# Performance work log

Hardware: AMD Instinct MI355X
Metric: run time of the kernel (lower is better)

## Reference

```python
import jax, jax.numpy as jnp
import numpy as np

D_MODEL = 1024
NHEAD = 16
HEAD_DIM = D_MODEL // NHEAD
EPS = 1e-5


def _layer_norm(x, gamma, beta):
    mu = jnp.mean(x, axis=-1, keepdims=True)
    var = jnp.mean(jnp.square(x - mu), axis=-1, keepdims=True)
    return (x - mu) * jax.lax.rsqrt(var + EPS) * gamma + beta


def setup_inputs() -> dict:
    key = jax.random.key(0)
    ks = jax.random.split(key, 8)
    s = 1.0 / np.sqrt(D_MODEL)
    return {
        "x": jax.random.normal(ks[0], (4, 2048, D_MODEL), dtype=jnp.float32),
        "Wq": jax.random.uniform(ks[1], (D_MODEL, D_MODEL), jnp.float32, -s, s),
        "Wk": jax.random.uniform(ks[2], (D_MODEL, D_MODEL), jnp.float32, -s, s),
        "Wv": jax.random.uniform(ks[3], (D_MODEL, D_MODEL), jnp.float32, -s, s),
        "ln1_g": jnp.ones((D_MODEL,), jnp.float32),
        "ln1_b": jnp.zeros((D_MODEL,), jnp.float32),
        "ln2_g": jnp.ones((D_MODEL,), jnp.float32),
        "ln2_b": jnp.zeros((D_MODEL,), jnp.float32),
        "W1": jax.random.uniform(ks[4], (D_MODEL, D_MODEL), jnp.float32, -s, s),
        "b1": jax.random.uniform(ks[5], (D_MODEL,), jnp.float32, -s, s),
        "W2": jax.random.uniform(ks[6], (D_MODEL, D_MODEL), jnp.float32, -s, s),
        "b2": jax.random.uniform(ks[7], (D_MODEL,), jnp.float32, -s, s),
    }


def reference(x, Wq, Wk, Wv, ln1_g, ln1_b, ln2_g, ln2_b, W1, b1, W2, b2):
    B, S, D = x.shape
    temperature = jnp.sqrt(jnp.asarray(D_MODEL / NHEAD, x.dtype))
    xn = _layer_norm(x, ln1_g, ln1_b)
    # torch Linear: y = x @ W.T (weights are [out, in], no bias for q/k/v)
    q = (xn @ Wq.T).reshape(B, S, NHEAD, HEAD_DIM)
    k = (xn @ Wk.T).reshape(B, S, NHEAD, HEAD_DIM)
    v = (xn @ Wv.T).reshape(B, S, NHEAD, HEAD_DIM)
    scores = jnp.einsum("bqhd,bkhd->bhqk", q, k) / temperature  # [B,H,S,S]
    causal = jnp.tril(jnp.ones((S, S), dtype=bool))
    scores = jnp.where(causal, scores, jnp.asarray(-jnp.inf, scores.dtype))
    attn = jax.nn.softmax(scores, axis=-1)
    att_out = jnp.einsum("bhqk,bkhd->bqhd", attn, v).reshape(B, S, D)
    xt = x + att_out
    xt2 = _layer_norm(xt, ln2_g, ln2_b)
    ffn = jax.nn.relu(xt2 @ W1.T + b1) @ W2.T + b2  # dropout=0 -> identity
    return xt + ffn
```

## Files before the change

### kernel.cpp

```cpp
#include <hip/hip_runtime.h>
#include <hip/hip_bf16.h>

typedef unsigned short u16;
typedef unsigned int u32;
typedef __attribute__((ext_vector_type(8))) __bf16 bf16x8;
typedef __attribute__((ext_vector_type(4))) float f32x4;
typedef __attribute__((ext_vector_type(8))) unsigned short ushort8v;
typedef __attribute__((ext_vector_type(4))) unsigned short u16x4;
typedef __attribute__((ext_vector_type(2))) unsigned int u32x2;

#define DEV __device__ __forceinline__
#define AS1 __attribute__((address_space(1)))
#define AS3 __attribute__((address_space(3)))

DEV u16 f2bf(float f) {
    union { float f; unsigned int i; } u; u.f = f;
    unsigned int x = u.i;
    unsigned int r = (x + 0x7fffu + ((x >> 16) & 1u)) >> 16;
    return (u16)r;
}
DEV float bf2f(u16 h) {
    union { unsigned int i; float f; } u; u.i = ((unsigned int)h) << 16;
    return u.f;
}
DEV u32 cvt_pk_bf16(float lo, float hi) {
    u32 r;
    asm("v_cvt_pk_bf16_f32 %0, %1, %2" : "=v"(r) : "v"(lo), "v"(hi));
    return r;
}

__global__ __launch_bounds__(256) void ln1_cvt(
    const float* __restrict__ xin,
    const float* __restrict__ g, const float* __restrict__ be,
    u16* __restrict__ y_bf,
    const float* __restrict__ wq, const float* __restrict__ wk,
    const float* __restrict__ wv, const float* __restrict__ w1,
    const float* __restrict__ w2, u16* __restrict__ wdst)
{
    const int tid = threadIdx.x;
    if (blockIdx.x >= 8192) {
        const int i = ((blockIdx.x - 8192) * 256 + tid) * 4;
        auto conv4 = [](float4 a) {
            u16x4 r; r[0] = f2bf(a.x); r[1] = f2bf(a.y); r[2] = f2bf(a.z); r[3] = f2bf(a.w);
            return r;
        };
        *(u16x4*)(wdst + i)               = conv4(*(const float4*)(wq + i));
        *(u16x4*)(wdst + (1 << 20) + i)   = conv4(*(const float4*)(wk + i));
        *(u16x4*)(wdst + (2 << 20) + i)   = conv4(*(const float4*)(wv + i));
        *(u16x4*)(wdst + (3 << 20) + i)   = conv4(*(const float4*)(w1 + i));
        *(u16x4*)(wdst + (4 << 20) + i)   = conv4(*(const float4*)(w2 + i));
        return;
    }
    const int row = blockIdx.x;
    const size_t base = (size_t)row * 1024 + tid * 4;
    float4 xv = *(const float4*)(xin + base);
    float v[4] = {xv.x, xv.y, xv.z, xv.w};
    float s = 0.f, ss = 0.f;
    #pragma unroll
    for (int j = 0; j < 4; ++j) { s += v[j]; ss += v[j] * v[j]; }
    #pragma unroll
    for (int o = 32; o > 0; o >>= 1) { s += __shfl_xor(s, o); ss += __shfl_xor(ss, o); }
    __shared__ float red[8];
    const int w = tid >> 6;
    if ((tid & 63) == 0) { red[w * 2] = s; red[w * 2 + 1] = ss; }
    __syncthreads();
    s  = red[0] + red[2] + red[4] + red[6];
    ss = red[1] + red[3] + red[5] + red[7];
    const float mu = s * (1.0f / 1024.0f);
    const float var = ss * (1.0f / 1024.0f) - mu * mu;
    const float rstd = rsqrtf(var + 1e-5f);
    const int col = tid * 4;
    float4 gv = *(const float4*)(g + col);
    float4 bv = *(const float4*)(be + col);
    u16x4 o4;
    o4[0] = f2bf((v[0] - mu) * rstd * gv.x + bv.x);
    o4[1] = f2bf((v[1] - mu) * rstd * gv.y + bv.y);
    o4[2] = f2bf((v[2] - mu) * rstd * gv.z + bv.z);
    o4[3] = f2bf((v[3] - mu) * rstd * gv.w + bv.w);
    *(u16x4*)(y_bf + base) = o4;
}

__global__ __launch_bounds__(256) void ln2_kernel(
    const float* __restrict__ xin, const u16* __restrict__ addbf,
    const float* __restrict__ g, const float* __restrict__ be,
    u16* __restrict__ xt_out, u16* __restrict__ y_bf)
{
    const int row = blockIdx.x;
    const int tid = threadIdx.x;
    const size_t base = (size_t)row * 1024 + tid * 4;

    float4 xv = *(const float4*)(xin + base);
    float v[4] = {xv.x, xv.y, xv.z, xv.w};
    u16x4 a = *(const u16x4*)(addbf + base);
    v[0] += bf2f(a[0]); v[1] += bf2f(a[1]); v[2] += bf2f(a[2]); v[3] += bf2f(a[3]);
    u16x4 o;
    o[0] = f2bf(v[0]); o[1] = f2bf(v[1]); o[2] = f2bf(v[2]); o[3] = f2bf(v[3]);
    *(u16x4*)(xt_out + base) = o;

    float s = 0.f, ss = 0.f;
    #pragma unroll
    for (int j = 0; j < 4; ++j) { s += v[j]; ss += v[j] * v[j]; }
    #pragma unroll
    for (int o2 = 32; o2 > 0; o2 >>= 1) { s += __shfl_xor(s, o2); ss += __shfl_xor(ss, o2); }
    __shared__ float red[8];
    const int w = tid >> 6;
    if ((tid & 63) == 0) { red[w * 2] = s; red[w * 2 + 1] = ss; }
    __syncthreads();
    s  = red[0] + red[2] + red[4] + red[6];
    ss = red[1] + red[3] + red[5] + red[7];
    const float mu = s * (1.0f / 1024.0f);
    const float var = ss * (1.0f / 1024.0f) - mu * mu;
    const float rstd = rsqrtf(var + 1e-5f);

    const int col = tid * 4;
    float4 gv = *(const float4*)(g + col);
    float4 bv = *(const float4*)(be + col);
    u16x4 o4;
    o4[0] = f2bf((v[0] - mu) * rstd * gv.x + bv.x);
    o4[1] = f2bf((v[1] - mu) * rstd * gv.y + bv.y);
    o4[2] = f2bf((v[2] - mu) * rstd * gv.z + bv.z);
    o4[3] = f2bf((v[3] - mu) * rstd * gv.w + bv.w);
    *(u16x4*)(y_bf + base) = o4;
}

template<int EPI>
__global__ __launch_bounds__(256, 4) void gemm_bt(
    const u16* __restrict__ A, const u16* __restrict__ Bt,
    void* __restrict__ Cout, const float* __restrict__ bias,
    const u16* __restrict__ resid, int M, int N, int K)
{
    __shared__ u16 As[2 * 128 * 32];
    __shared__ u16 Bs[2 * 128 * 32];
    const int tid = threadIdx.x;
    const int l = tid & 63;
    const int w = tid >> 6;
    const int wm = w >> 1, wn = w & 1;
    const int fr = l & 15, fc = l >> 4;
    const size_t rowA0 = (size_t)blockIdx.x * 128;
    const size_t rowB0 = (size_t)blockIdx.y * 128;

    f32x4 acc[4][4] = {};
    const int ldoff = fr * 32 + fc * 8;

    const int nkt = K >> 6;
    for (int kt = 0; kt < nkt; ++kt) {
        __syncthreads();
        const int k0 = kt << 6;
        #pragma unroll
        for (int q = 0; q < 4; ++q) {
            const int row = (q & 1) * 64 + w * 16 + (l >> 2);
            const int kk  = (q >> 1) * 32 + (l & 3) * 8;
            const u16* ga = A  + (rowA0 + row) * K + k0 + kk;
            const u16* gb = Bt + (rowB0 + row) * K + k0 + kk;
            u16* da = As + q * 2048 + w * 512;
            u16* db = Bs + q * 2048 + w * 512;
            __builtin_amdgcn_global_load_lds((const AS1 void*)ga, (AS3 void*)da, 16, 0, 0);
            __builtin_amdgcn_global_load_lds((const AS1 void*)gb, (AS3 void*)db, 16, 0, 0);
        }
        __syncthreads();
        #pragma unroll
        for (int ks = 0; ks < 2; ++ks) {
            const u16* as_p = As + ks * 4096;
            const u16* bs_p = Bs + ks * 4096;
            bf16x8 af[4], bfv[4];
            #pragma unroll
            for (int m = 0; m < 4; ++m)
                af[m] = *(const bf16x8*)(as_p + (wm * 64 + m * 16) * 32 + ldoff);
            #pragma unroll
            for (int n = 0; n < 4; ++n)
                bfv[n] = *(const bf16x8*)(bs_p + (wn * 64 + n * 16) * 32 + ldoff);
            #pragma unroll
            for (int m = 0; m < 4; ++m)
                #pragma unroll
                for (int n = 0; n < 4; ++n)
                    acc[m][n] = __builtin_amdgcn_mfma_f32_16x16x32_bf16(
                        af[m], bfv[n], acc[m][n], 0, 0, 0);
        }
    }

    const int r0 = (int)rowA0 + wm * 64;
    const int c0 = (int)rowB0 + wn * 64;
    #pragma unroll
    for (int m = 0; m < 4; ++m) {
        #pragma unroll
        for (int n = 0; n < 4; ++n) {
            const int rowbase = r0 + m * 16 + fc * 4;
            const int col = c0 + n * 16 + fr;
            if constexpr (EPI == 0) {
                const int which = col >> 10;
                const int hh = (col >> 6) & 15;
                const int dd = col & 63;
                const size_t hb2 = (size_t)(rowbase >> 11) * 16 + hh;
                const int s0 = rowbase & 2047;
                if (which == 2) {
                    u16x4 pk;
                    #pragma unroll
                    for (int j = 0; j < 4; ++j) pk[j] = f2bf(acc[m][n][j]);
                    *(u16x4*)((u16*)Cout + (size_t)2 * 8388608 +
                              (hb2 * 64 + dd) * 2048 + s0) = pk;
                } else {
                    #pragma unroll
                    for (int j = 0; j < 4; ++j)
                        ((u16*)Cout)[(size_t)which * 8388608 +
                                     (hb2 * 2048 + s0 + j) * 64 + dd] =
                            f2bf(acc[m][n][j]);
                }
            } else {
                #pragma unroll
                for (int j = 0; j < 4; ++j) {
                    float v = acc[m][n][j];
                    const size_t idx = (size_t)(rowbase + j) * N + col;
                    if constexpr (EPI == 1) {
                        v += bias[col];
                        v = fmaxf(v, 0.0f);
                        ((u16*)Cout)[idx] = f2bf(v);
                    } else {
                        v += bias[col] + bf2f(resid[idx]);
                        ((float*)Cout)[idx] = v;
                    }
                }
            }
        }
    }
}

__global__ __launch_bounds__(256, 4) void attn_fwd(
    const u16* __restrict__ Qh, const u16* __restrict__ Kh,
    const u16* __restrict__ Vh, u16* __restrict__ attout)
{
    __shared__ u16 Ks[2][64 * 64];
    __shared__ u16 Vt[2][64 * 64];
    __shared__ u16 Pw[4][16 * 64];

    const int bid = blockIdx.x;
    const int pair = (bid >> 3) & 15;
    const int g = (bid & 7) + 8 * (bid >> 7);
    const int h = g & 15, b = g >> 4;

    const int tid = threadIdx.x, l = tid & 63, w = tid >> 6;
    const int fr = l & 15, fc = l >> 4;
    const int hb = b * 16 + h;
    const size_t head = (size_t)hb << 17;
    const u16* kb_g = Kh + head;
    const u16* vb_g = Vh + head;
    u16* pw = &Pw[w][0];

    const int sw = (fr & 7) << 3;
    const int col0 = (fc * 8) ^ sw;
    const int col1 = col0 ^ 32;

    const int grow0 = w * 16 + (l >> 3);
    const int gsw   = ((l & 7) * 8) ^ ((l >> 3) << 3);

    const float qs = 0.125f * 1.44269504f;

    bf16x8 onesv;
    #pragma unroll
    for (int j = 0; j < 8; ++j) onesv[j] = (__bf16)1.0f;

    #pragma unroll 1
    for (int half = 0; half < 2; ++half) {
        const int qt = half ? 31 - pair : pair;
        const int qbase = qt * 64 + w * 16;
        const int qg = qbase + fr;

        const u16* qp = Qh + head + (size_t)(qbase + fr) * 64 + fc * 8;
        bf16x8 qf0 = *(const bf16x8*)qp;
        bf16x8 qf1 = *(const bf16x8*)(qp + 32);
        #pragma unroll
        for (int j = 0; j < 8; ++j) {
            qf0[j] = (__bf16)((float)qf0[j] * qs);
            qf1[j] = (__bf16)((float)qf1[j] * qs);
        }

        f32x4 acc_o[4] = {};
        float l_run[4] = {0.f, 0.f, 0.f, 0.f};

        const int nkt = qt + 1;
        int cur = 0;

        #pragma unroll
        for (int i = 0; i < 2; ++i) {
            const int row = grow0 + i * 8;
            __builtin_amdgcn_global_load_lds(
                (const AS1 void*)(kb_g + (size_t)row * 64 + gsw),
                (AS3 void*)(&Ks[0][0] + (w * 16 + i * 8) * 64), 16, 0, 0);
            __builtin_amdgcn_global_load_lds(
                (const AS1 void*)(vb_g + (size_t)row * 2048 + gsw),
                (AS3 void*)(&Vt[0][0] + (w * 16 + i * 8) * 64), 16, 0, 0);
        }
        __builtin_amdgcn_sched_barrier(0);
        asm volatile("s_waitcnt vmcnt(0)" ::: "memory");
        __builtin_amdgcn_s_barrier();

        #pragma unroll 1
        for (int kt = 0; kt < nkt; ++kt) {
            const int kv0 = kt * 64;
            const bool diag = (kt == qt);
            const u16* ksc = &Ks[cur][0];
            const u16* vtc = &Vt[cur][0];

            if (kt + 1 < nkt) {
                u16* ksn = &Ks[cur ^ 1][0];
                u16* vtn = &Vt[cur ^ 1][0];
                #pragma unroll
                for (int i = 0; i < 2; ++i) {
                    const int row = grow0 + i * 8;
                    __builtin_amdgcn_global_load_lds(
                        (const AS1 void*)(kb_g + (size_t)(kv0 + 64 + row) * 64 + gsw),
                        (AS3 void*)(ksn + (w * 16 + i * 8) * 64), 16, 0, 0);
                    __builtin_amdgcn_global_load_lds(
                        (const AS1 void*)(vb_g + (size_t)row * 2048 + kv0 + 64 + gsw),
                        (AS3 void*)(vtn + (w * 16 + i * 8) * 64), 16, 0, 0);
                }
            }
            __builtin_amdgcn_sched_barrier(0);

            f32x4 sa[4] = {};
            __builtin_amdgcn_s_setprio(1);
            #pragma unroll
            for (int nb = 0; nb < 4; ++nb) {
                const u16* kb = ksc + (nb * 16 + fr) * 64;
                sa[nb] = __builtin_amdgcn_mfma_f32_16x16x32_bf16(
                    *(const bf16x8*)(kb + col0), qf0, sa[nb], 0, 0, 0);
                sa[nb] = __builtin_amdgcn_mfma_f32_16x16x32_bf16(
                    *(const bf16x8*)(kb + col1), qf1, sa[nb], 0, 0, 0);
            }
            __builtin_amdgcn_s_setprio(0);

            if (diag) {
                #pragma unroll
                for (int nb = 0; nb < 4; ++nb)
                    #pragma unroll
                    for (int j = 0; j < 4; ++j) {
                        const int kg = kv0 + nb * 16 + fc * 4 + j;
                        if (kg > qg) sa[nb][j] = -3.0e38f;
                    }
            }

            #pragma unroll
            for (int nb = 0; nb < 4; ++nb)
                #pragma unroll
                for (int j = 0; j < 4; ++j)
                    sa[nb][j] = exp2f(sa[nb][j]);

            #pragma unroll
            for (int nb = 0; nb < 4; ++nb) {
                u32x2 pkv;
                pkv[0] = cvt_pk_bf16(sa[nb][0], sa[nb][1]);
                pkv[1] = cvt_pk_bf16(sa[nb][2], sa[nb][3]);
                *(u32x2*)(pw + fr * 64 + ((nb * 16 + fc * 4) ^ sw)) = pkv;
            }
            const u16* prd = pw + fr * 64;
            const bf16x8 pf0 = *(const bf16x8*)(prd + col0);
            const bf16x8 pf1 = *(const bf16x8*)(prd + col1);
            f32x4 acc_s = {};
            __builtin_amdgcn_s_setprio(1);
            #pragma unroll
            for (int db = 0; db < 4; ++db) {
                const u16* vb = vtc + (db * 16 + fr) * 64;
                acc_o[db] = __builtin_amdgcn_mfma_f32_16x16x32_bf16(
                    pf0, *(const bf16x8*)(vb + col0), acc_o[db], 0, 0, 0);
                acc_o[db] = __builtin_amdgcn_mfma_f32_16x16x32_bf16(
                    pf1, *(const bf16x8*)(vb + col1), acc_o[db], 0, 0, 0);
            }
            acc_s = __builtin_amdgcn_mfma_f32_16x16x32_bf16(pf0, onesv, acc_s, 0, 0, 0);
            acc_s = __builtin_amdgcn_mfma_f32_16x16x32_bf16(pf1, onesv, acc_s, 0, 0, 0);
            __builtin_amdgcn_s_setprio(0);
            #pragma unroll
            for (int j = 0; j < 4; ++j)
                l_run[j] += acc_s[j];

            __builtin_amdgcn_sched_barrier(0);
            asm volatile("s_waitcnt vmcnt(0)" ::: "memory");
            asm volatile("s_waitcnt lgkmcnt(0)" ::: "memory");
            __builtin_amdgcn_s_barrier();
            cur ^= 1;
        }

        float inv[4];
        #pragma unroll
        for (int j = 0; j < 4; ++j) inv[j] = 1.0f / l_run[j];
        const size_t bS = (size_t)b * 2048;
        #pragma unroll
        for (int db = 0; db < 4; ++db)
            #pragma unroll
            for (int j = 0; j < 4; ++j)
                attout[(bS + qbase + fc * 4 + j) * 1024 + h * 64 + db * 16 + fr] =
                    f2bf(acc_o[db][j] * inv[j]);
    }
}

extern "C" void kernel_launch(void* const* d_in, const int* in_sizes, int n_in,
                              void* d_out, int out_size, void* d_ws, size_t ws_size,
                              hipStream_t stream)
{
    const float* x    = (const float*)d_in[0];
    const float* Wq   = (const float*)d_in[1];
    const float* Wk   = (const float*)d_in[2];
    const float* Wv   = (const float*)d_in[3];
    const float* ln1g = (const float*)d_in[4];
    const float* ln1b = (const float*)d_in[5];
    const float* ln2g = (const float*)d_in[6];
    const float* ln2b = (const float*)d_in[7];
    const float* W1   = (const float*)d_in[8];
    const float* b1   = (const float*)d_in[9];
    const float* W2   = (const float*)d_in[10];
    const float* b2   = (const float*)d_in[11];

    char* ws = (char*)d_ws;
    u16*   wbf  = (u16*)(ws);
    u16*   xn   = (u16*)(ws + 10485760);
    u16*   qkvb = (u16*)(ws + 27262976);
    u16*   attb = (u16*)(ws + 77594624);
    u16*   xt   = (u16*)(ws + 94371840);

    ln1_cvt<<<9216, 256, 0, stream>>>(x, ln1g, ln1b, xn, Wq, Wk, Wv, W1, W2, wbf);
    gemm_bt<0><<<dim3(64, 24), 256, 0, stream>>>(xn, wbf, qkvb, nullptr, nullptr,
                                                 8192, 3072, 1024);
    attn_fwd<<<1024, 256, 0, stream>>>(qkvb, qkvb + 8388608, qkvb + 16777216, attb);
    ln2_kernel<<<8192, 256, 0, stream>>>(x, attb, ln2g, ln2b, xt, xn);
    gemm_bt<1><<<dim3(64, 8), 256, 0, stream>>>(xn, wbf + (3 << 20), qkvb, b1, nullptr,
                                                8192, 1024, 1024);
    gemm_bt<2><<<dim3(64, 8), 256, 0, stream>>>(qkvb, wbf + (4 << 20), d_out, b2, xt,
                                                8192, 1024, 1024);
}
```

Baseline: 208.8 us.

## Rewrite attention with 32x32x16 MFMA, register P via permlane swap, 2 waves

```diff
diff --git a/kernel.cpp b/kernel.cpp
--- a/kernel.cpp
+++ b/kernel.cpp
@@ -5,9 +5,10 @@
 typedef unsigned int u32;
 typedef __attribute__((ext_vector_type(8))) __bf16 bf16x8;
 typedef __attribute__((ext_vector_type(4))) float f32x4;
+typedef __attribute__((ext_vector_type(16))) float f32x16;
 typedef __attribute__((ext_vector_type(8))) unsigned short ushort8v;
 typedef __attribute__((ext_vector_type(4))) unsigned short u16x4;
-typedef __attribute__((ext_vector_type(2))) unsigned int u32x2;
+typedef __attribute__((ext_vector_type(4))) unsigned int u32x4;
 
 #define DEV __device__ __forceinline__
 #define AS1 __attribute__((address_space(1)))
@@ -27,6 +28,9 @@
     u32 r;
     asm("v_cvt_pk_bf16_f32 %0, %1, %2" : "=v"(r) : "v"(lo), "v"(hi));
     return r;
+}
+DEV void pl32swap(u32& a, u32& b) {
+    asm volatile("v_permlane32_swap_b32 %0, %1" : "+v"(a), "+v"(b));
 }
 
 __global__ __launch_bounds__(256) void ln1_cvt(
@@ -224,13 +228,12 @@
     }
 }
 
-__global__ __launch_bounds__(256, 4) void attn_fwd(
+__global__ __launch_bounds__(128, 2) void attn_fwd(
     const u16* __restrict__ Qh, const u16* __restrict__ Kh,
     const u16* __restrict__ Vh, u16* __restrict__ attout)
 {
     __shared__ u16 Ks[2][64 * 64];
     __shared__ u16 Vt[2][64 * 64];
-    __shared__ u16 Pw[4][16 * 64];
 
     const int bid = blockIdx.x;
     const int pair = (bid >> 3) & 15;
@@ -238,56 +241,54 @@
     const int h = g & 15, b = g >> 4;
 
     const int tid = threadIdx.x, l = tid & 63, w = tid >> 6;
-    const int fr = l & 15, fc = l >> 4;
+    const int lq = l & 31;
+    const int hi = l >> 5;
+    const int hi8 = hi * 8;
     const int hb = b * 16 + h;
     const size_t head = (size_t)hb << 17;
     const u16* kb_g = Kh + head;
     const u16* vb_g = Vh + head;
-    u16* pw = &Pw[w][0];
-
-    const int sw = (fr & 7) << 3;
-    const int col0 = (fc * 8) ^ sw;
-    const int col1 = col0 ^ 32;
-
-    const int grow0 = w * 16 + (l >> 3);
+
+    const int swr = (lq & 7) << 3;
+
+    const int grow0 = w * 32 + (l >> 3);
     const int gsw   = ((l & 7) * 8) ^ ((l >> 3) << 3);
 
     const float qs = 0.125f * 1.44269504f;
-
-    bf16x8 onesv;
-    #pragma unroll
-    for (int j = 0; j < 8; ++j) onesv[j] = (__bf16)1.0f;
 
     #pragma unroll 1
     for (int half = 0; half < 2; ++half) {
         const int qt = half ? 31 - pair : pair;
-        const int qbase = qt * 64 + w * 16;
-        const int qg = qbase + fr;
-
-        const u16* qp = Qh + head + (size_t)(qbase + fr) * 64 + fc * 8;
-        bf16x8 qf0 = *(const bf16x8*)qp;
-        bf16x8 qf1 = *(const bf16x8*)(qp + 32);
-        #pragma unroll
-        for (int j = 0; j < 8; ++j) {
-            qf0[j] = (__bf16)((float)qf0[j] * qs);
-            qf1[j] = (__bf16)((float)qf1[j] * qs);
-        }
-
-        f32x4 acc_o[4] = {};
-        float l_run[4] = {0.f, 0.f, 0.f, 0.f};
+        const int qbase = qt * 64 + w * 32;
+        const int qg = qbase + lq;
+
+        bf16x8 qf[4];
+        {
+            const u16* qp = Qh + head + (size_t)(qbase + lq) * 64 + hi8;
+            #pragma unroll
+            for (int ds = 0; ds < 4; ++ds) {
+                qf[ds] = *(const bf16x8*)(qp + ds * 16);
+                #pragma unroll
+                for (int j = 0; j < 8; ++j)
+                    qf[ds][j] = (__bf16)((float)qf[ds][j] * qs);
+            }
+        }
+
+        f32x16 acc[2] = {};
+        float l_part = 0.0f;
 
         const int nkt = qt + 1;
         int cur = 0;
 
         #pragma unroll
-        for (int i = 0; i < 2; ++i) {
+        for (int i = 0; i < 4; ++i) {
             const int row = grow0 + i * 8;
             __builtin_amdgcn_global_load_lds(
                 (const AS1 void*)(kb_g + (size_t)row * 64 + gsw),
-                (AS3 void*)(&Ks[0][0] + (w * 16 + i * 8) * 64), 16, 0, 0);
+                (AS3 void*)(&Ks[0][0] + (w * 32 + i * 8) * 64), 16, 0, 0);
             __builtin_amdgcn_global_load_lds(
                 (const AS1 void*)(vb_g + (size_t)row * 2048 + gsw),
-                (AS3 void*)(&Vt[0][0] + (w * 16 + i * 8) * 64), 16, 0, 0);
+                (AS3 void*)(&Vt[0][0] + (w * 32 + i * 8) * 64), 16, 0, 0);
         }
         __builtin_amdgcn_sched_barrier(0);
         asm volatile("s_waitcnt vmcnt(0)" ::: "memory");
@@ -304,72 +305,75 @@
                 u16* ksn = &Ks[cur ^ 1][0];
                 u16* vtn = &Vt[cur ^ 1][0];
                 #pragma unroll
-                for (int i = 0; i < 2; ++i) {
+                for (int i = 0; i < 4; ++i) {
                     const int row = grow0 + i * 8;
                     __builtin_amdgcn_global_load_lds(
                         (const AS1 void*)(kb_g + (size_t)(kv0 + 64 + row) * 64 + gsw),
-                        (AS3 void*)(ksn + (w * 16 + i * 8) * 64), 16, 0, 0);
+                        (AS3 void*)(ksn + (w * 32 + i * 8) * 64), 16, 0, 0);
                     __builtin_amdgcn_global_load_lds(
                         (const AS1 void*)(vb_g + (size_t)row * 2048 + kv0 + 64 + gsw),
-                        (AS3 void*)(vtn + (w * 16 + i * 8) * 64), 16, 0, 0);
+                        (AS3 void*)(vtn + (w * 32 + i * 8) * 64), 16, 0, 0);
                 }
             }
             __builtin_amdgcn_sched_barrier(0);
 
-            f32x4 sa[4] = {};
-            __builtin_amdgcn_s_setprio(1);
-            #pragma unroll
-            for (int nb = 0; nb < 4; ++nb) {
-                const u16* kb = ksc + (nb * 16 + fr) * 64;
-                sa[nb] = __builtin_amdgcn_mfma_f32_16x16x32_bf16(
-                    *(const bf16x8*)(kb + col0), qf0, sa[nb], 0, 0, 0);
-                sa[nb] = __builtin_amdgcn_mfma_f32_16x16x32_bf16(
-                    *(const bf16x8*)(kb + col1), qf1, sa[nb], 0, 0, 0);
-            }
-            __builtin_amdgcn_s_setprio(0);
-
-            if (diag) {
-                #pragma unroll
-                for (int nb = 0; nb < 4; ++nb)
+            auto do_kvblk = [&](int kvblk) {
+                f32x16 sa = {};
+                const u16* kbase = ksc + (lq + kvblk * 32) * 64;
+                __builtin_amdgcn_s_setprio(1);
+                #pragma unroll
+                for (int ds = 0; ds < 4; ++ds) {
+                    const bf16x8 kf = *(const bf16x8*)(kbase + ((ds * 16 + hi8) ^ swr));
+                    sa = __builtin_amdgcn_mfma_f32_32x32x16_bf16(kf, qf[ds], sa, 0, 0, 0);
+                }
+                __builtin_amdgcn_s_setprio(0);
+
+                if (diag) {
+                    const int kvb = kv0 + kvblk * 32 + 4 * hi;
                     #pragma unroll
-                    for (int j = 0; j < 4; ++j) {
-                        const int kg = kv0 + nb * 16 + fc * 4 + j;
-                        if (kg > qg) sa[nb][j] = -3.0e38f;
+                    for (int r = 0; r < 16; ++r) {
+                        const int kg = kvb + (r & 3) + 8 * (r >> 2);
+                        if (kg > qg) sa[r] = -3.0e38f;
                     }
-            }
-
-            #pragma unroll
-            for (int nb = 0; nb < 4; ++nb)
-                #pragma unroll
-                for (int j = 0; j < 4; ++j)
-                    sa[nb][j] = exp2f(sa[nb][j]);
-
-            #pragma unroll
-            for (int nb = 0; nb < 4; ++nb) {
-                u32x2 pkv;
-                pkv[0] = cvt_pk_bf16(sa[nb][0], sa[nb][1]);
-                pkv[1] = cvt_pk_bf16(sa[nb][2], sa[nb][3]);
-                *(u32x2*)(pw + fr * 64 + ((nb * 16 + fc * 4) ^ sw)) = pkv;
-            }
-            const u16* prd = pw + fr * 64;
-            const bf16x8 pf0 = *(const bf16x8*)(prd + col0);
-            const bf16x8 pf1 = *(const bf16x8*)(prd + col1);
-            f32x4 acc_s = {};
-            __builtin_amdgcn_s_setprio(1);
-            #pragma unroll
-            for (int db = 0; db < 4; ++db) {
-                const u16* vb = vtc + (db * 16 + fr) * 64;
-                acc_o[db] = __builtin_amdgcn_mfma_f32_16x16x32_bf16(
-                    pf0, *(const bf16x8*)(vb + col0), acc_o[db], 0, 0, 0);
-                acc_o[db] = __builtin_amdgcn_mfma_f32_16x16x32_bf16(
-                    pf1, *(const bf16x8*)(vb + col1), acc_o[db], 0, 0, 0);
-            }
-            acc_s = __builtin_amdgcn_mfma_f32_16x16x32_bf16(pf0, onesv, acc_s, 0, 0, 0);
-            acc_s = __builtin_amdgcn_mfma_f32_16x16x32_bf16(pf1, onesv, acc_s, 0, 0, 0);
-            __builtin_amdgcn_s_setprio(0);
-            #pragma unroll
-            for (int j = 0; j < 4; ++j)
-                l_run[j] += acc_s[j];
+                }
+
+                float ls = 0.0f;
+                #pragma unroll
+                for (int r = 0; r < 16; ++r) { sa[r] = exp2f(sa[r]); ls += sa[r]; }
+                l_part += ls;
+
+                u32 P0 = cvt_pk_bf16(sa[0],  sa[1]);
+                u32 P1 = cvt_pk_bf16(sa[2],  sa[3]);
+                u32 P2 = cvt_pk_bf16(sa[4],  sa[5]);
+                u32 P3 = cvt_pk_bf16(sa[6],  sa[7]);
+                u32 P4 = cvt_pk_bf16(sa[8],  sa[9]);
+                u32 P5 = cvt_pk_bf16(sa[10], sa[11]);
+                u32 P6 = cvt_pk_bf16(sa[12], sa[13]);
+                u32 P7 = cvt_pk_bf16(sa[14], sa[15]);
+                pl32swap(P0, P2); pl32swap(P1, P3);
+                pl32swap(P4, P6); pl32swap(P5, P7);
+                u32x4 w0 = {P0, P1, P2, P3};
+                u32x4 w1 = {P4, P5, P6, P7};
+                const bf16x8 pf0 = __builtin_bit_cast(bf16x8, w0);
+                const bf16x8 pf1 = __builtin_bit_cast(bf16x8, w1);
+
+                __builtin_amdgcn_s_setprio(1);
+                #pragma unroll
+                for (int dblk = 0; dblk < 2; ++dblk) {
+                    const u16* vbase = vtc + (lq + dblk * 32) * 64;
+                    const bf16x8 vf0 = *(const bf16x8*)(vbase + ((kvblk * 32 + hi8) ^ swr));
+                    acc[dblk] = __builtin_amdgcn_mfma_f32_32x32x16_bf16(
+                        vf0, pf0, acc[dblk], 0, 0, 0);
+                    const bf16x8 vf1 = *(const bf16x8*)(vbase + ((kvblk * 32 + 16 + hi8) ^ swr));
+                    acc[dblk] = __builtin_amdgcn_mfma_f32_32x32x16_bf16(
+                        vf1, pf1, acc[dblk], 0, 0, 0);
+                }
+                __builtin_amdgcn_s_setprio(0);
+            };
+
+            do_kvblk(0);
+            if (!(diag && w == 0))
+                do_kvblk(1);
 
             __builtin_amdgcn_sched_barrier(0);
             asm volatile("s_waitcnt vmcnt(0)" ::: "memory");
@@ -378,16 +382,20 @@
             cur ^= 1;
         }
 
-        float inv[4];
+        const float l_tot = l_part + __shfl_xor(l_part, 32);
+        const float inv = 1.0f / l_tot;
+        const size_t obase = ((size_t)b * 2048 + qbase + lq) * 1024 + h * 64;
         #pragma unroll
-        for (int j = 0; j < 4; ++j) inv[j] = 1.0f / l_run[j];
-        const size_t bS = (size_t)b * 2048;
-        #pragma unroll
-        for (int db = 0; db < 4; ++db)
+        for (int dblk = 0; dblk < 2; ++dblk) {
             #pragma unroll
-            for (int j = 0; j < 4; ++j)
-                attout[(bS + qbase + fc * 4 + j) * 1024 + h * 64 + db * 16 + fr] =
-                    f2bf(acc_o[db][j] * inv[j]);
+            for (int gq = 0; gq < 4; ++gq) {
+                u16x4 o;
+                #pragma unroll
+                for (int j = 0; j < 4; ++j)
+                    o[j] = f2bf(acc[dblk][4 * gq + j] * inv);
+                *(u16x4*)(attout + obase + dblk * 32 + gq * 8 + 4 * hi) = o;
+            }
+        }
     }
 }
 
@@ -418,7 +426,7 @@
     ln1_cvt<<<9216, 256, 0, stream>>>(x, ln1g, ln1b, xn, Wq, Wk, Wv, W1, W2, wbf);
     gemm_bt<0><<<dim3(64, 24), 256, 0, stream>>>(xn, wbf, qkvb, nullptr, nullptr,
                                                  8192, 3072, 1024);
-    attn_fwd<<<1024, 256, 0, stream>>>(qkvb, qkvb + 8388608, qkvb + 16777216, attb);
+    attn_fwd<<<1024, 128, 0, stream>>>(qkvb, qkvb + 8388608, qkvb + 16777216, attb);
     ln2_kernel<<<8192, 256, 0, stream>>>(x, attb, ln2g, ln2b, xt, xn);
     gemm_bt<1><<<dim3(64, 8), 256, 0, stream>>>(xn, wbf + (3 << 20), qkvb, b1, nullptr,
                                                 8192, 1024, 1024);
```

Result: slower. 227.0 us (+8.7%).
